# Optimization experiments

Hardware: AMD Instinct MI355X
Metric: run time of the kernel (lower is better)

The kernel has to match this reference:

```python
import jax, jax.numpy as jnp
import numpy as np
from jax import lax


def setup_inputs() -> dict:
    key = jax.random.key(0)
    ks = jax.random.split(key, 8)
    B, S, V, E, H, O = 64, 200, 50000, 300, 512, 5
    return {
        "x": jax.random.randint(ks[0], (B, S), 0, V),
        "emb": jax.random.normal(ks[1], (V, E), dtype=jnp.float32),
        "W_ih": jax.random.normal(ks[2], (4 * H, E), dtype=jnp.float32) * 0.05,
        "W_hh": jax.random.normal(ks[3], (4 * H, H), dtype=jnp.float32) * 0.05,
        "b_ih": jax.random.normal(ks[4], (4 * H,), dtype=jnp.float32) * 0.05,
        "b_hh": jax.random.normal(ks[5], (4 * H,), dtype=jnp.float32) * 0.05,
        "W_fc": jax.random.normal(ks[6], (O, H), dtype=jnp.float32) * 0.05,
        "b_fc": jax.random.normal(ks[7], (O,), dtype=jnp.float32) * 0.05,
        "batch_size": B,
    }


def reference(x, emb, W_ih, W_hh, b_ih, b_hh, W_fc, b_fc, batch_size):
    H = W_hh.shape[1]
    B = x.shape[0]
    vec = jnp.transpose(emb[x], (1, 0, 2))  # [S, B, E] (time-major, as nn.LSTM)
    b = b_ih + b_hh  # [4H]

    def step(carry, xt):
        h, c = carry
        gates = xt @ W_ih.T + h @ W_hh.T + b  # [B, 4H]
        i, f, g, o = jnp.split(gates, 4, axis=-1)  # PyTorch gate order i,f,g,o
        i = jax.nn.sigmoid(i)
        f = jax.nn.sigmoid(f)
        g = jnp.tanh(g)
        o = jax.nn.sigmoid(o)
        c = f * c + i * g
        h = o * jnp.tanh(c)
        return (h, c), None

    h0 = jnp.zeros((B, H), dtype=vec.dtype)
    c0 = jnp.zeros((B, H), dtype=vec.dtype)
    (h_final, _), _ = lax.scan(step, (h0, c0), vec)
    logits = h_final @ W_fc.T + b_fc  # [B, O]
    return jax.nn.softmax(logits, axis=-1)
```

## Files before the change

kernel.cpp:

```cpp
#include <hip/hip_runtime.h>

#define TPB   256
#define NWG   512
#define SEQL  200
#define BATCH 64
#define EDIM  300
#define HDIM  512
#define ODIM  5
#define NROW  (4*HDIM)

#define GROUPS 16
#define GCUS   32
#define GB     4
#define UNITS  16
#define KSLC   32

#define EX_OFF   2048
#define EX_RSTR  69
#define EX_BSTR  17
#define EMB_OFF  (EX_OFF + 64*EX_RSTR)
#define LDS_BYTES 56320

#define HT_GROUP 2048
#define HT_PAR   (GROUPS * HT_GROUP)
#define HT_BYTES (2 * HT_PAR * 8)

#define ESTR 308
#define PRE_LDS_BYTES (BATCH * ESTR * 4)

#define GATES_FLOATS ((size_t)SEQL * NROW * BATCH)

__device__ __forceinline__ float fast_sigmoid(float x) {
    return 1.0f / (1.0f + __expf(-x));
}
__device__ __forceinline__ float fast_tanh(float x) {
    return 2.0f / (1.0f + __expf(-2.0f * x)) - 1.0f;
}

extern "C" __global__ void __launch_bounds__(256, 1)
lstm_pre(const int* __restrict__ x, const float* __restrict__ emb,
         const float* __restrict__ W_ih, float* __restrict__ gates)
{
    extern __shared__ float embs[];
    const int tid = threadIdx.x;
    const int s   = blockIdx.x >> 3;
    const int rb  = blockIdx.x & 7;

    for (int i = tid; i < BATCH * 75; i += 256) {
        int b = i / 75, jj = i - b * 75;
        int row = x[b * SEQL + s];
        float4 v = ((const float4*)(emb + (size_t)row * EDIM))[jj];
        *(float4*)&embs[b * ESTR + 4 * jj] = v;
    }
    __syncthreads();

    const int bi = tid >> 5;
    const int ri = tid & 31;
    const int row0 = rb * 256 + ri * 8;
    const float* wp = W_ih + (size_t)row0 * EDIM;

    float acc[8][8];
#pragma unroll
    for (int a = 0; a < 8; a++)
#pragma unroll
        for (int b = 0; b < 8; b++) acc[a][b] = 0.0f;

    for (int t2 = 0; t2 < 75; t2++) {
        float4 w[8], e[8];
#pragma unroll
        for (int rr = 0; rr < 8; rr++)
            w[rr] = *(const float4*)(wp + rr * EDIM + 4 * t2);
#pragma unroll
        for (int bb = 0; bb < 8; bb++)
            e[bb] = *(const float4*)&embs[(bi * 8 + bb) * ESTR + 4 * t2];
#pragma unroll
        for (int rr = 0; rr < 8; rr++)
#pragma unroll
            for (int bb = 0; bb < 8; bb++) {
                acc[rr][bb] = fmaf(w[rr].x, e[bb].x, acc[rr][bb]);
                acc[rr][bb] = fmaf(w[rr].y, e[bb].y, acc[rr][bb]);
                acc[rr][bb] = fmaf(w[rr].z, e[bb].z, acc[rr][bb]);
                acc[rr][bb] = fmaf(w[rr].w, e[bb].w, acc[rr][bb]);
            }
    }
    float* dstA = gates + (size_t)(s * GROUPS + 2 * bi)     * 8192 + row0 * 4;
    float* dstB = gates + (size_t)(s * GROUPS + 2 * bi + 1) * 8192 + row0 * 4;
#pragma unroll
    for (int rr = 0; rr < 8; rr++) {
        *(float4*)(dstA + 4 * rr) = make_float4(acc[rr][0], acc[rr][1], acc[rr][2], acc[rr][3]);
        *(float4*)(dstB + 4 * rr) = make_float4(acc[rr][4], acc[rr][5], acc[rr][6], acc[rr][7]);
    }
}

extern "C" __global__ void __launch_bounds__(TPB, 2)
lstm_persist(const int* __restrict__ x, const float* __restrict__ emb,
             const float* __restrict__ W_ih, const float* __restrict__ W_hh,
             const float* __restrict__ b_ih, const float* __restrict__ b_hh,
             const float* __restrict__ gates,
             unsigned long long* __restrict__ htag)
{
    extern __shared__ float lds[];
    const int tid = threadIdx.x;
    const int g   = blockIdx.x & 15;
    const int j   = blockIdx.x >> 4;
    const bool pre = (gates != nullptr);

    const int rq = tid & 15;
    const int kh = tid >> 4;
    const int wv = tid >> 6;
    const int ln = tid & 63;

    float4 w4[4][8];
#pragma unroll
    for (int p = 0; p < 4; p++) {
        const int r = 4 * rq + p;
        const size_t R = (size_t)((r >> 4) * HDIM + UNITS * j + (r & 15));
        const float* wp = W_hh + R * HDIM + KSLC * kh;
#pragma unroll
        for (int kq = 0; kq < 8; kq++) w4[p][kq] = *(const float4*)(wp + 4 * kq);
    }
#pragma unroll
    for (int p = 0; p < 4; p++)
#pragma unroll
        for (int kq = 0; kq < 8; kq++)
            asm volatile("" : "+v"(w4[p][kq].x), "+v"(w4[p][kq].y),
                             "+v"(w4[p][kq].z), "+v"(w4[p][kq].w));

    const int uu = (tid & 63) >> 2;
    const int cb = tid & 3;
    float bias4[4];
#pragma unroll
    for (int gt = 0; gt < 4; gt++) {
        int R = gt * HDIM + UNITS * j + uu;
        bias4[gt] = b_ih[R] + b_hh[R];
    }
    float c_reg = 0.0f;

    const int swz = (kh & 3) << 2;

    unsigned long long* const T0 = htag + (size_t)g * HT_GROUP;
    unsigned long long* const T1 = htag + HT_PAR + (size_t)g * HT_GROUP;

    __syncthreads();

    for (int s = 0; s < SEQL; s++) {
        const unsigned long long* Tin = (s & 1) ? T1 : T0;
        unsigned long long*       Tout = (s & 1) ? T0 : T1;

        float gp[4] = {0.f, 0.f, 0.f, 0.f};
        if (pre && tid < 64) {
            const float* gbase = gates + (size_t)(s * GROUPS + g) * 8192 + 64 * j;
#pragma unroll
            for (int gt = 0; gt < 4; gt++)
                gp[gt] = __builtin_nontemporal_load(gbase + gt * 2048 + tid);
        }

        float acc[4][4];
#pragma unroll
        for (int p = 0; p < 4; p++)
#pragma unroll
            for (int b = 0; b < 4; b++) acc[p][b] = 0.f;

        if (!pre) {
            for (int i = tid; i < EDIM * GB; i += TPB) {
                int e = i >> 2, b = i & 3;
                int row = x[(GB * g + b) * SEQL + s];
                lds[EMB_OFF + i] = emb[(size_t)row * EDIM + e];
            }
            __syncthreads();
            if (kh < 15) {
                for (int e = 20 * kh; e < 20 * kh + 20; e++) {
                    float4 e0 = *(const float4*)&lds[EMB_OFF + 4 * e];
#pragma unroll
                    for (int p = 0; p < 4; p++) {
                        const int r = 4 * rq + p;
                        const size_t R = (size_t)((r >> 4) * HDIM + UNITS * j + (r & 15));
                        float wc = W_ih[R * EDIM + e];
                        acc[p][0] = fmaf(wc, e0.x, acc[p][0]);
                        acc[p][1] = fmaf(wc, e0.y, acc[p][1]);
                        acc[p][2] = fmaf(wc, e0.z, acc[p][2]);
                        acc[p][3] = fmaf(wc, e0.w, acc[p][3]);
                    }
                }
            }
            __syncthreads();
        }

        {
            const unsigned tag = (unsigned)s;
#pragma unroll
            for (int rr = 0; rr < 2; rr++) {
                const int k = 128 * wv + 64 * rr + ln;
                const int vi = 4 * k;
                unsigned long long d0, d1, d2, d3;
                for (;;) {
                    d0 = __hip_atomic_load(Tin + vi + 0, __ATOMIC_RELAXED, __HIP_MEMORY_SCOPE_AGENT);
                    d1 = __hip_atomic_load(Tin + vi + 1, __ATOMIC_RELAXED, __HIP_MEMORY_SCOPE_AGENT);
                    d2 = __hip_atomic_load(Tin + vi + 2, __ATOMIC_RELAXED, __HIP_MEMORY_SCOPE_AGENT);
                    d3 = __hip_atomic_load(Tin + vi + 3, __ATOMIC_RELAXED, __HIP_MEMORY_SCOPE_AGENT);
                    if ((unsigned)(d0 >> 32) == tag && (unsigned)(d1 >> 32) == tag &&
                        (unsigned)(d2 >> 32) == tag && (unsigned)(d3 >> 32) == tag)
                        break;
                    __builtin_amdgcn_s_sleep(1);
                }
                const int phys = (4 * k) ^ (((k >> 5) & 3) << 2);
                float4 hv;
                hv.x = __uint_as_float((unsigned)d0);
                hv.y = __uint_as_float((unsigned)d1);
                hv.z = __uint_as_float((unsigned)d2);
                hv.w = __uint_as_float((unsigned)d3);
                *(float4*)&lds[phys] = hv;
            }
        }
        asm volatile("" ::: "memory");

#pragma unroll
        for (int kq = 0; kq < 8; kq++) {
#pragma unroll
            for (int ki = 0; ki < 4; ki++) {
                const int kidx = 4 * kq + ki;
                const float4 h0 = *(const float4*)&lds[128 * kh + ((4 * kidx) ^ swz)];
#pragma unroll
                for (int p = 0; p < 4; p++) {
                    const float4 wvv = w4[p][kq];
                    const float wc = ki == 0 ? wvv.x : ki == 1 ? wvv.y
                                   : ki == 2 ? wvv.z : wvv.w;
                    acc[p][0] = fmaf(wc, h0.x, acc[p][0]);
                    acc[p][1] = fmaf(wc, h0.y, acc[p][1]);
                    acc[p][2] = fmaf(wc, h0.z, acc[p][2]);
                    acc[p][3] = fmaf(wc, h0.w, acc[p][3]);
                }
            }
        }

#pragma unroll
        for (int p = 0; p < 4; p++) {
            const int base = EX_OFF + (4 * rq + p) * EX_RSTR + kh;
#pragma unroll
            for (int b = 0; b < 4; b++)
                lds[base + b * EX_BSTR] = acc[p][b];
        }
        __syncthreads();

        if (tid < 64) {
            float gs[4];
#pragma unroll
            for (int gt = 0; gt < 4; gt++) {
                float sum = bias4[gt] + gp[gt];
                const int base = EX_OFF + (gt * 16 + uu) * EX_RSTR + cb * EX_BSTR;
#pragma unroll
                for (int kk = 0; kk < 16; kk++) sum += lds[base + kk];
                gs[gt] = sum;
            }
            float iv = fast_sigmoid(gs[0]);
            float fv = fast_sigmoid(gs[1]);
            float gv = fast_tanh(gs[2]);
            float ov = fast_sigmoid(gs[3]);
            c_reg = fv * c_reg + iv * gv;
            float hv = ov * fast_tanh(c_reg);
            unsigned long long wword =
                ((unsigned long long)(unsigned)(s + 1) << 32) |
                (unsigned long long)__float_as_uint(hv);
            __hip_atomic_store(Tout + 64 * j + tid, wword,
                               __ATOMIC_RELAXED, __HIP_MEMORY_SCOPE_AGENT);
        }
        __syncthreads();
    }
}

extern "C" __global__ void __launch_bounds__(320)
lstm_epilogue(const unsigned long long* __restrict__ htag,
              const float* __restrict__ W_fc, const float* __restrict__ b_fc,
              float* __restrict__ out)
{
    __shared__ float sl[ODIM * BATCH];
    const int t = threadIdx.x;
    {
        int o = t / BATCH, b = t - o * BATCH;
        const unsigned long long* hb = htag + (size_t)(b >> 2) * HT_GROUP;
        const int bc = b & 3;
        float acc = b_fc[o];
        const float4* wv = (const float4*)(W_fc + o * HDIM);
#pragma unroll 8
        for (int k4 = 0; k4 < HDIM / 4; k4++) {
            float4 w = wv[k4];
            const int k0 = 4 * k4;
            acc = fmaf(__uint_as_float((unsigned)hb[(k0 + 0) * 4 + bc]), w.x, acc);
            acc = fmaf(__uint_as_float((unsigned)hb[(k0 + 1) * 4 + bc]), w.y, acc);
            acc = fmaf(__uint_as_float((unsigned)hb[(k0 + 2) * 4 + bc]), w.z, acc);
            acc = fmaf(__uint_as_float((unsigned)hb[(k0 + 3) * 4 + bc]), w.w, acc);
        }
        sl[o * BATCH + b] = acc;
    }
    __syncthreads();
    if (t < BATCH) {
        float l0 = sl[t], l1 = sl[BATCH + t], l2 = sl[2 * BATCH + t];
        float l3 = sl[3 * BATCH + t], l4 = sl[4 * BATCH + t];
        float m = fmaxf(fmaxf(fmaxf(l0, l1), fmaxf(l2, l3)), l4);
        float e0 = __expf(l0 - m), e1 = __expf(l1 - m), e2 = __expf(l2 - m);
        float e3 = __expf(l3 - m), e4 = __expf(l4 - m);
        float inv = 1.0f / (e0 + e1 + e2 + e3 + e4);
        out[t * ODIM + 0] = e0 * inv;
        out[t * ODIM + 1] = e1 * inv;
        out[t * ODIM + 2] = e2 * inv;
        out[t * ODIM + 3] = e3 * inv;
        out[t * ODIM + 4] = e4 * inv;
    }
}

extern "C" void kernel_launch(void* const* d_in, const int* in_sizes, int n_in,
                              void* d_out, int out_size, void* d_ws, size_t ws_size,
                              hipStream_t stream)
{
    const int*   x    = (const int*)d_in[0];
    const float* emb  = (const float*)d_in[1];
    const float* W_ih = (const float*)d_in[2];
    const float* W_hh = (const float*)d_in[3];
    const float* b_ih = (const float*)d_in[4];
    const float* b_hh = (const float*)d_in[5];
    const float* W_fc = (const float*)d_in[6];
    const float* b_fc = (const float*)d_in[7];
    float* out = (float*)d_out;

    unsigned long long* htag = (unsigned long long*)d_ws;
    const size_t gates_bytes = GATES_FLOATS * sizeof(float);
    float* gates = nullptr;
    if (ws_size >= (size_t)HT_BYTES + gates_bytes)
        gates = (float*)((char*)d_ws + HT_BYTES);

    (void)hipMemsetAsync(htag, 0, HT_BYTES, stream);

    (void)hipFuncSetAttribute((const void*)lstm_persist,
                              hipFuncAttributeMaxDynamicSharedMemorySize, LDS_BYTES);
    if (gates) {
        (void)hipFuncSetAttribute((const void*)lstm_pre,
                                  hipFuncAttributeMaxDynamicSharedMemorySize, PRE_LDS_BYTES);
        lstm_pre<<<SEQL * 8, 256, PRE_LDS_BYTES, stream>>>(x, emb, W_ih, gates);
    }

    lstm_persist<<<NWG, TPB, LDS_BYTES, stream>>>(x, emb, W_ih, W_hh, b_ih, b_hh,
                                                  gates, htag);

    lstm_epilogue<<<1, 320, 0, stream>>>(htag, W_fc, b_fc, out);
}
```

Measured before the change: 1.732 ms.

## Remap K-split across lanes with shuffle reduction and double-buffered exchange

Thread mapping changes so each quad of lanes splits the K dimension for one hidden unit, and partial sums are reduced with xor shuffles instead of a 16-way LDS exchange. The exchange buffer is double-buffered by step parity, which removes the trailing __syncthreads per timestep. The gate epilogue is spread across all four wavefronts (16 lanes each) instead of the first wave only. The aim is less LDS traffic and one fewer barrier on the serial recurrence critical path, at the cost of changed LDS access patterns and swizzle.

```diff
diff --git a/kernel.cpp b/kernel.cpp
--- a/kernel.cpp
+++ b/kernel.cpp
@@ -13,12 +13,9 @@
 #define GCUS   32
 #define GB     4
 #define UNITS  16
-#define KSLC   32
 
 #define EX_OFF   2048
-#define EX_RSTR  69
-#define EX_BSTR  17
-#define EMB_OFF  (EX_OFF + 64*EX_RSTR)
+#define EMB_OFF  4096
 #define LDS_BYTES 56320
 
 #define HT_GROUP 2048
@@ -105,38 +102,36 @@
     const int j   = blockIdx.x >> 4;
     const bool pre = (gates != nullptr);
 
-    const int rq = tid & 15;
-    const int kh = tid >> 4;
     const int wv = tid >> 6;
-    const int ln = tid & 63;
+    const int l  = tid & 63;
+    const int u  = l >> 2;
+    const int kq = l & 3;
+    const int kbase = 128 * wv + 32 * kq;
 
     float4 w4[4][8];
 #pragma unroll
     for (int p = 0; p < 4; p++) {
-        const int r = 4 * rq + p;
-        const size_t R = (size_t)((r >> 4) * HDIM + UNITS * j + (r & 15));
-        const float* wp = W_hh + R * HDIM + KSLC * kh;
-#pragma unroll
-        for (int kq = 0; kq < 8; kq++) w4[p][kq] = *(const float4*)(wp + 4 * kq);
+        const size_t R = (size_t)(p * HDIM + UNITS * j + u);
+        const float* wp = W_hh + R * HDIM + kbase;
+#pragma unroll
+        for (int q = 0; q < 8; q++) w4[p][q] = *(const float4*)(wp + 4 * q);
     }
 #pragma unroll
     for (int p = 0; p < 4; p++)
 #pragma unroll
-        for (int kq = 0; kq < 8; kq++)
-            asm volatile("" : "+v"(w4[p][kq].x), "+v"(w4[p][kq].y),
-                             "+v"(w4[p][kq].z), "+v"(w4[p][kq].w));
-
-    const int uu = (tid & 63) >> 2;
-    const int cb = tid & 3;
+        for (int q = 0; q < 8; q++)
+            asm volatile("" : "+v"(w4[p][q].x), "+v"(w4[p][q].y),
+                             "+v"(w4[p][q].z), "+v"(w4[p][q].w));
+
+    const int cu = 4 * wv + ((l >> 2) & 3);
+    const int cb = l & 3;
     float bias4[4];
 #pragma unroll
     for (int gt = 0; gt < 4; gt++) {
-        int R = gt * HDIM + UNITS * j + uu;
+        int R = gt * HDIM + UNITS * j + cu;
         bias4[gt] = b_ih[R] + b_hh[R];
     }
     float c_reg = 0.0f;
-
-    const int swz = (kh & 3) << 2;
 
     unsigned long long* const T0 = htag + (size_t)g * HT_GROUP;
     unsigned long long* const T1 = htag + HT_PAR + (size_t)g * HT_GROUP;
@@ -146,13 +141,14 @@
     for (int s = 0; s < SEQL; s++) {
         const unsigned long long* Tin = (s & 1) ? T1 : T0;
         unsigned long long*       Tout = (s & 1) ? T0 : T1;
+        const int par = s & 1;
 
         float gp[4] = {0.f, 0.f, 0.f, 0.f};
-        if (pre && tid < 64) {
-            const float* gbase = gates + (size_t)(s * GROUPS + g) * 8192 + 64 * j;
+        if (pre && l < 16) {
+            const float* gbase = gates + (size_t)(s * GROUPS + g) * 8192;
 #pragma unroll
             for (int gt = 0; gt < 4; gt++)
-                gp[gt] = __builtin_nontemporal_load(gbase + gt * 2048 + tid);
+                gp[gt] = __builtin_nontemporal_load(gbase + gt * 2048 + 64 * j + 4 * cu + cb);
         }
 
         float acc[4][4];
@@ -168,19 +164,17 @@
                 lds[EMB_OFF + i] = emb[(size_t)row * EDIM + e];
             }
             __syncthreads();
-            if (kh < 15) {
-                for (int e = 20 * kh; e < 20 * kh + 20; e++) {
-                    float4 e0 = *(const float4*)&lds[EMB_OFF + 4 * e];
-#pragma unroll
-                    for (int p = 0; p < 4; p++) {
-                        const int r = 4 * rq + p;
-                        const size_t R = (size_t)((r >> 4) * HDIM + UNITS * j + (r & 15));
-                        float wc = W_ih[R * EDIM + e];
-                        acc[p][0] = fmaf(wc, e0.x, acc[p][0]);
-                        acc[p][1] = fmaf(wc, e0.y, acc[p][1]);
-                        acc[p][2] = fmaf(wc, e0.z, acc[p][2]);
-                        acc[p][3] = fmaf(wc, e0.w, acc[p][3]);
-                    }
+            const int sl = 4 * wv + kq;
+            const int e0 = 19 * sl, e1 = (19 * sl + 19 < EDIM) ? 19 * sl + 19 : EDIM;
+            for (int e = e0; e < e1; e++) {
+                float4 ev = *(const float4*)&lds[EMB_OFF + 4 * e];
+#pragma unroll
+                for (int p = 0; p < 4; p++) {
+                    float wc = W_ih[(size_t)(p * HDIM + UNITS * j + u) * EDIM + e];
+                    acc[p][0] = fmaf(wc, ev.x, acc[p][0]);
+                    acc[p][1] = fmaf(wc, ev.y, acc[p][1]);
+                    acc[p][2] = fmaf(wc, ev.z, acc[p][2]);
+                    acc[p][3] = fmaf(wc, ev.w, acc[p][3]);
                 }
             }
             __syncthreads();
@@ -190,7 +184,7 @@
             const unsigned tag = (unsigned)s;
 #pragma unroll
             for (int rr = 0; rr < 2; rr++) {
-                const int k = 128 * wv + 64 * rr + ln;
+                const int k = 128 * wv + 2 * l + rr;
                 const int vi = 4 * k;
                 unsigned long long d0, d1, d2, d3;
                 for (;;) {
@@ -213,16 +207,17 @@
             }
         }
         asm volatile("" ::: "memory");
-
-#pragma unroll
-        for (int kq = 0; kq < 8; kq++) {
+        __builtin_amdgcn_sched_barrier(0);
+
+#pragma unroll
+        for (int q = 0; q < 8; q++) {
 #pragma unroll
             for (int ki = 0; ki < 4; ki++) {
-                const int kidx = 4 * kq + ki;
-                const float4 h0 = *(const float4*)&lds[128 * kh + ((4 * kidx) ^ swz)];
+                const int k = kbase + 4 * q + ki;
+                const float4 h0 = *(const float4*)&lds[(4 * k) ^ (kq << 2)];
 #pragma unroll
                 for (int p = 0; p < 4; p++) {
-                    const float4 wvv = w4[p][kq];
+                    const float4 wvv = w4[p][q];
                     const float wc = ki == 0 ? wvv.x : ki == 1 ? wvv.y
                                    : ki == 2 ? wvv.z : wvv.w;
                     acc[p][0] = fmaf(wc, h0.x, acc[p][0]);
@@ -234,23 +229,30 @@
         }
 
 #pragma unroll
-        for (int p = 0; p < 4; p++) {
-            const int base = EX_OFF + (4 * rq + p) * EX_RSTR + kh;
-#pragma unroll
-            for (int b = 0; b < 4; b++)
-                lds[base + b * EX_BSTR] = acc[p][b];
+        for (int p = 0; p < 4; p++)
+#pragma unroll
+            for (int b = 0; b < 4; b++) {
+                acc[p][b] += __shfl_xor(acc[p][b], 1);
+                acc[p][b] += __shfl_xor(acc[p][b], 2);
+            }
+
+        if (kq == 0) {
+            const int base = EX_OFF + par * 1024 + wv * 256 + u;
+#pragma unroll
+            for (int p = 0; p < 4; p++)
+#pragma unroll
+                for (int b = 0; b < 4; b++)
+                    lds[base + p * 64 + b * 16] = acc[p][b];
         }
         __syncthreads();
 
-        if (tid < 64) {
+        if (l < 16) {
             float gs[4];
 #pragma unroll
             for (int gt = 0; gt < 4; gt++) {
-                float sum = bias4[gt] + gp[gt];
-                const int base = EX_OFF + (gt * 16 + uu) * EX_RSTR + cb * EX_BSTR;
-#pragma unroll
-                for (int kk = 0; kk < 16; kk++) sum += lds[base + kk];
-                gs[gt] = sum;
+                const int base = EX_OFF + par * 1024 + gt * 64 + cb * 16 + cu;
+                gs[gt] = bias4[gt] + gp[gt]
+                       + lds[base] + lds[base + 256] + lds[base + 512] + lds[base + 768];
             }
             float iv = fast_sigmoid(gs[0]);
             float fv = fast_sigmoid(gs[1]);
@@ -261,10 +263,9 @@
             unsigned long long wword =
                 ((unsigned long long)(unsigned)(s + 1) << 32) |
                 (unsigned long long)__float_as_uint(hv);
-            __hip_atomic_store(Tout + 64 * j + tid, wword,
+            __hip_atomic_store(Tout + 64 * j + 4 * cu + cb, wword,
                                __ATOMIC_RELAXED, __HIP_MEMORY_SCOPE_AGENT);
         }
-        __syncthreads();
     }
 }
 
```

Result: slower. 1.958 ms (+13.0%).

## Fuse input projection into persistent LSTM kernel with register-resident W_ih

Applied to the files above, without the earlier changes.

Removes the separate lstm_pre GEMM and its large gates buffer, so each persistent workgroup now computes the input projection for its own rows every step. The W_ih slice is kept in registers (wih[4][5]) next to the register-held W_hh. The per-step embedding gather is split across waves and its syncthreads pairs are dropped. This saves the pre-kernel time and the global gate traffic, at the cost of extra per-step FMAs and a gather on the serial critical path, plus higher register pressure at two workgroups per CU.

```diff
diff --git a/kernel.cpp b/kernel.cpp
--- a/kernel.cpp
+++ b/kernel.cpp
@@ -7,124 +7,69 @@
 #define EDIM  300
 #define HDIM  512
 #define ODIM  5
-#define NROW  (4*HDIM)
 
 #define GROUPS 16
-#define GCUS   32
 #define GB     4
 #define UNITS  16
-#define KSLC   32
 
 #define EX_OFF   2048
 #define EX_RSTR  69
 #define EX_BSTR  17
-#define EMB_OFF  (EX_OFF + 64*EX_RSTR)
+#define EMB_OFF  6464
 #define LDS_BYTES 56320
 
 #define HT_GROUP 2048
 #define HT_PAR   (GROUPS * HT_GROUP)
 #define HT_BYTES (2 * HT_PAR * 8)
 
-#define ESTR 308
-#define PRE_LDS_BYTES (BATCH * ESTR * 4)
-
-#define GATES_FLOATS ((size_t)SEQL * NROW * BATCH)
-
 __device__ __forceinline__ float fast_sigmoid(float x) {
     return 1.0f / (1.0f + __expf(-x));
 }
 __device__ __forceinline__ float fast_tanh(float x) {
     return 2.0f / (1.0f + __expf(-2.0f * x)) - 1.0f;
-}
-
-extern "C" __global__ void __launch_bounds__(256, 1)
-lstm_pre(const int* __restrict__ x, const float* __restrict__ emb,
-         const float* __restrict__ W_ih, float* __restrict__ gates)
-{
-    extern __shared__ float embs[];
-    const int tid = threadIdx.x;
-    const int s   = blockIdx.x >> 3;
-    const int rb  = blockIdx.x & 7;
-
-    for (int i = tid; i < BATCH * 75; i += 256) {
-        int b = i / 75, jj = i - b * 75;
-        int row = x[b * SEQL + s];
-        float4 v = ((const float4*)(emb + (size_t)row * EDIM))[jj];
-        *(float4*)&embs[b * ESTR + 4 * jj] = v;
-    }
-    __syncthreads();
-
-    const int bi = tid >> 5;
-    const int ri = tid & 31;
-    const int row0 = rb * 256 + ri * 8;
-    const float* wp = W_ih + (size_t)row0 * EDIM;
-
-    float acc[8][8];
-#pragma unroll
-    for (int a = 0; a < 8; a++)
-#pragma unroll
-        for (int b = 0; b < 8; b++) acc[a][b] = 0.0f;
-
-    for (int t2 = 0; t2 < 75; t2++) {
-        float4 w[8], e[8];
-#pragma unroll
-        for (int rr = 0; rr < 8; rr++)
-            w[rr] = *(const float4*)(wp + rr * EDIM + 4 * t2);
-#pragma unroll
-        for (int bb = 0; bb < 8; bb++)
-            e[bb] = *(const float4*)&embs[(bi * 8 + bb) * ESTR + 4 * t2];
-#pragma unroll
-        for (int rr = 0; rr < 8; rr++)
-#pragma unroll
-            for (int bb = 0; bb < 8; bb++) {
-                acc[rr][bb] = fmaf(w[rr].x, e[bb].x, acc[rr][bb]);
-                acc[rr][bb] = fmaf(w[rr].y, e[bb].y, acc[rr][bb]);
-                acc[rr][bb] = fmaf(w[rr].z, e[bb].z, acc[rr][bb]);
-                acc[rr][bb] = fmaf(w[rr].w, e[bb].w, acc[rr][bb]);
-            }
-    }
-    float* dstA = gates + (size_t)(s * GROUPS + 2 * bi)     * 8192 + row0 * 4;
-    float* dstB = gates + (size_t)(s * GROUPS + 2 * bi + 1) * 8192 + row0 * 4;
-#pragma unroll
-    for (int rr = 0; rr < 8; rr++) {
-        *(float4*)(dstA + 4 * rr) = make_float4(acc[rr][0], acc[rr][1], acc[rr][2], acc[rr][3]);
-        *(float4*)(dstB + 4 * rr) = make_float4(acc[rr][4], acc[rr][5], acc[rr][6], acc[rr][7]);
-    }
 }
 
 extern "C" __global__ void __launch_bounds__(TPB, 2)
 lstm_persist(const int* __restrict__ x, const float* __restrict__ emb,
              const float* __restrict__ W_ih, const float* __restrict__ W_hh,
              const float* __restrict__ b_ih, const float* __restrict__ b_hh,
-             const float* __restrict__ gates,
              unsigned long long* __restrict__ htag)
 {
     extern __shared__ float lds[];
     const int tid = threadIdx.x;
     const int g   = blockIdx.x & 15;
     const int j   = blockIdx.x >> 4;
-    const bool pre = (gates != nullptr);
-
-    const int rq = tid & 15;
-    const int kh = tid >> 4;
-    const int wv = tid >> 6;
-    const int ln = tid & 63;
+    const int rq  = tid & 15;
+    const int kh  = tid >> 4;
+    const int wv  = tid >> 6;
+    const int ln  = tid & 63;
 
     float4 w4[4][8];
 #pragma unroll
     for (int p = 0; p < 4; p++) {
         const int r = 4 * rq + p;
         const size_t R = (size_t)((r >> 4) * HDIM + UNITS * j + (r & 15));
-        const float* wp = W_hh + R * HDIM + KSLC * kh;
+        const float* wp = W_hh + R * HDIM + 32 * kh;
 #pragma unroll
         for (int kq = 0; kq < 8; kq++) w4[p][kq] = *(const float4*)(wp + 4 * kq);
     }
+
+    float4 wih[4][5];
 #pragma unroll
     for (int p = 0; p < 4; p++)
 #pragma unroll
-        for (int kq = 0; kq < 8; kq++)
-            asm volatile("" : "+v"(w4[p][kq].x), "+v"(w4[p][kq].y),
-                             "+v"(w4[p][kq].z), "+v"(w4[p][kq].w));
+        for (int eq = 0; eq < 5; eq++)
+            wih[p][eq] = make_float4(0.f, 0.f, 0.f, 0.f);
+    if (kh < 15) {
+#pragma unroll
+        for (int p = 0; p < 4; p++) {
+            const int r = 4 * rq + p;
+            const size_t R = (size_t)((r >> 4) * HDIM + UNITS * j + (r & 15));
+            const float* wp = W_ih + R * EDIM + 20 * kh;
+#pragma unroll
+            for (int eq = 0; eq < 5; eq++) wih[p][eq] = *(const float4*)(wp + 4 * eq);
+        }
+    }
 
     const int uu = (tid & 63) >> 2;
     const int cb = tid & 3;
@@ -147,43 +92,41 @@
         const unsigned long long* Tin = (s & 1) ? T1 : T0;
         unsigned long long*       Tout = (s & 1) ? T0 : T1;
 
-        float gp[4] = {0.f, 0.f, 0.f, 0.f};
-        if (pre && tid < 64) {
-            const float* gbase = gates + (size_t)(s * GROUPS + g) * 8192 + 64 * j;
-#pragma unroll
-            for (int gt = 0; gt < 4; gt++)
-                gp[gt] = __builtin_nontemporal_load(gbase + gt * 2048 + tid);
-        }
-
         float acc[4][4];
 #pragma unroll
         for (int p = 0; p < 4; p++)
 #pragma unroll
             for (int b = 0; b < 4; b++) acc[p][b] = 0.f;
 
-        if (!pre) {
-            for (int i = tid; i < EDIM * GB; i += TPB) {
-                int e = i >> 2, b = i & 3;
-                int row = x[(GB * g + b) * SEQL + s];
-                lds[EMB_OFF + i] = emb[(size_t)row * EDIM + e];
-            }
-            __syncthreads();
+        {
+            const int b = ln & 3;
+            const int row = x[(GB * g + b) * SEQL + s];
+            const float* ebase = emb + (size_t)row * EDIM;
+            const int i1 = (wv == 3) ? (EDIM * GB) : 320 * wv + 320;
+            for (int i = 320 * wv + ln; i < i1; i += 64)
+                lds[EMB_OFF + i] = ebase[i >> 2];
+            asm volatile("" ::: "memory");
+            __builtin_amdgcn_sched_barrier(0);
             if (kh < 15) {
-                for (int e = 20 * kh; e < 20 * kh + 20; e++) {
-                    float4 e0 = *(const float4*)&lds[EMB_OFF + 4 * e];
-#pragma unroll
-                    for (int p = 0; p < 4; p++) {
-                        const int r = 4 * rq + p;
-                        const size_t R = (size_t)((r >> 4) * HDIM + UNITS * j + (r & 15));
-                        float wc = W_ih[R * EDIM + e];
-                        acc[p][0] = fmaf(wc, e0.x, acc[p][0]);
-                        acc[p][1] = fmaf(wc, e0.y, acc[p][1]);
-                        acc[p][2] = fmaf(wc, e0.z, acc[p][2]);
-                        acc[p][3] = fmaf(wc, e0.w, acc[p][3]);
+#pragma unroll
+                for (int eq = 0; eq < 5; eq++) {
+#pragma unroll
+                    for (int ei = 0; ei < 4; ei++) {
+                        const int e = 20 * kh + 4 * eq + ei;
+                        const float4 ev = *(const float4*)&lds[EMB_OFF + 4 * e];
+#pragma unroll
+                        for (int p = 0; p < 4; p++) {
+                            const float4 wvv = wih[p][eq];
+                            const float wc = ei == 0 ? wvv.x : ei == 1 ? wvv.y
+                                           : ei == 2 ? wvv.z : wvv.w;
+                            acc[p][0] = fmaf(wc, ev.x, acc[p][0]);
+                            acc[p][1] = fmaf(wc, ev.y, acc[p][1]);
+                            acc[p][2] = fmaf(wc, ev.z, acc[p][2]);
+                            acc[p][3] = fmaf(wc, ev.w, acc[p][3]);
+                        }
                     }
                 }
             }
-            __syncthreads();
         }
 
         {
@@ -213,6 +156,7 @@
             }
         }
         asm volatile("" ::: "memory");
+        __builtin_amdgcn_sched_barrier(0);
 
 #pragma unroll
         for (int kq = 0; kq < 8; kq++) {
@@ -246,7 +190,7 @@
             float gs[4];
 #pragma unroll
             for (int gt = 0; gt < 4; gt++) {
-                float sum = bias4[gt] + gp[gt];
+                float sum = bias4[gt];
                 const int base = EX_OFF + (gt * 16 + uu) * EX_RSTR + cb * EX_BSTR;
 #pragma unroll
                 for (int kk = 0; kk < 16; kk++) sum += lds[base + kk];
@@ -323,23 +267,13 @@
     float* out = (float*)d_out;
 
     unsigned long long* htag = (unsigned long long*)d_ws;
-    const size_t gates_bytes = GATES_FLOATS * sizeof(float);
-    float* gates = nullptr;
-    if (ws_size >= (size_t)HT_BYTES + gates_bytes)
-        gates = (float*)((char*)d_ws + HT_BYTES);
-
     (void)hipMemsetAsync(htag, 0, HT_BYTES, stream);
 
     (void)hipFuncSetAttribute((const void*)lstm_persist,
                               hipFuncAttributeMaxDynamicSharedMemorySize, LDS_BYTES);
-    if (gates) {
-        (void)hipFuncSetAttribute((const void*)lstm_pre,
-                                  hipFuncAttributeMaxDynamicSharedMemorySize, PRE_LDS_BYTES);
-        lstm_pre<<<SEQL * 8, 256, PRE_LDS_BYTES, stream>>>(x, emb, W_ih, gates);
-    }
-
-    lstm_persist<<<NWG, TPB, LDS_BYTES, stream>>>(x, emb, W_ih, W_hh, b_ih, b_hh,
-                                                  gates, htag);
+
+    lstm_persist<<<NWG, TPB, LDS_BYTES, stream>>>(x, emb, W_ih, W_hh,
+                                                  b_ih, b_hh, htag);
 
     lstm_epilogue<<<1, 320, 0, stream>>>(htag, W_fc, b_fc, out);
 }
```

New measurement: 3.414 ms. 97.1% more time.
